# Performance work log

Hardware: AMD Instinct MI355X
Metric: run time of the kernel (lower is better)

## Reference

```python
import jax, jax.numpy as jnp
import numpy as np

B, C, H, W = 4, 128, 128, 128
NCLS = 80
NCONV = 2


def conv3x3(x, w, b):
    # x: [B,Cin,H,W], w: [Cout,Cin,3,3]
    y = jax.lax.conv_general_dilated(x, w, (1, 1), 'SAME',
                                     dimension_numbers=('NCHW', 'OIHW', 'NCHW'))
    return y + b[None, :, None, None]


def setup_inputs() -> dict:
    key = jax.random.key(0)
    ks = jax.random.split(key, 10)
    std = 0.01  # conv init std in the torch module
    prior_prob = 0.01
    bias_value = -np.log((1 - prior_prob) / prior_prob)
    inp = {
        'feature': jax.random.normal(ks[0], (B, C, H, W), jnp.float32),
        'targets': jax.random.uniform(ks[1], (B, NCLS, H, W), jnp.float32),
        'cls_w': std * jax.random.normal(ks[2], (NCONV, C, C, 3, 3), jnp.float32),
        'cls_b': jnp.zeros((NCONV, C), jnp.float32),
        'bbox_w': std * jax.random.normal(ks[3], (NCONV, C, C, 3, 3), jnp.float32),
        'bbox_b': jnp.zeros((NCONV, C), jnp.float32),
        'off_w': std * jax.random.normal(ks[4], (NCONV, C, C, 3, 3), jnp.float32),
        'off_b': jnp.zeros((NCONV, C), jnp.float32),
        'cls_score_w': std * jax.random.normal(ks[5], (NCLS, C, 3, 3), jnp.float32),
        'cls_score_b': jnp.full((NCLS,), bias_value, jnp.float32),
        'bbox_pred_w': std * jax.random.normal(ks[6], (2, C, 3, 3), jnp.float32),
        'bbox_pred_b': jnp.zeros((2,), jnp.float32),
        'center_off_w': std * jax.random.normal(ks[7], (2, C, 3, 3), jnp.float32),
        'center_off_b': jnp.zeros((2,), jnp.float32),
        'K': 100,
    }
    return inp


def centernet_forward(feature, targets, cls_w, cls_b, bbox_w, bbox_b, off_w, off_b,
                      cls_score_w, cls_score_b, bbox_pred_w, bbox_pred_b,
                      center_off_w, center_off_b, K):
    # ---- head: three conv+ReLU subnets + final 3x3 heads ----
    xc, xb, xo = feature, feature, feature
    for i in range(NCONV):
        xc = jax.nn.relu(conv3x3(xc, cls_w[i], cls_b[i]))
        xb = jax.nn.relu(conv3x3(xb, bbox_w[i], bbox_b[i]))
        xo = jax.nn.relu(conv3x3(xo, off_w[i], off_b[i]))
    logits = conv3x3(xc, cls_score_w, cls_score_b)      # [B,NCLS,H,W]
    wh = conv3x3(xb, bbox_pred_w, bbox_pred_b)          # [B,2,H,W]
    off = conv3x3(xo, center_off_w, center_off_b)       # [B,2,H,W]

    # ---- center focal loss (alpha=2, beta=4, reduction='sum') ----
    pos = (targets == 1.0).astype(logits.dtype)
    neg = (targets < 1.0).astype(logits.dtype)
    neg_w = jnp.power(1.0 - targets, 4.0)
    p = jax.nn.sigmoid(logits)
    log_p = jax.nn.log_sigmoid(logits)        # log(sigmoid(x))
    log_1mp = jax.nn.log_sigmoid(-logits)     # log(1 - sigmoid(x))
    pos_loss = log_p * jnp.square(1.0 - p) * pos
    neg_loss = log_1mp * jnp.square(p) * neg_w * neg
    loss = -(pos_loss.sum()) - (neg_loss.sum())

    # ---- decode: sigmoid + 3x3 maxpool pseudo-NMS + top-k + gather ----
    hm = p  # sigmoid heatmap
    hmax = jax.lax.reduce_window(hm, -jnp.inf, jax.lax.max,
                                 (1, 1, 3, 3), (1, 1, 1, 1), 'SAME')
    hm_nms = jnp.where(hmax == hm, hm, 0.0)
    scores, inds = jax.lax.top_k(hm_nms.reshape(B, -1), K)  # [B,K]
    hw = H * W
    clses = inds // hw                 # [B,K] int class ids
    sp = inds % hw                     # spatial index
    ys = (sp // W).astype(jnp.float32)
    xs = (sp % W).astype(jnp.float32)
    # gather wh/offset at peak locations
    wh_k = jnp.take_along_axis(wh.reshape(B, 2, hw), sp[:, None, :], axis=2)    # [B,2,K]
    off_k = jnp.take_along_axis(off.reshape(B, 2, hw), sp[:, None, :], axis=2)  # [B,2,K]
    cx = xs + off_k[:, 0]
    cy = ys + off_k[:, 1]
    w_, h_ = wh_k[:, 0], wh_k[:, 1]
    boxes = jnp.stack([cx - w_ / 2, cy - h_ / 2, cx + w_ / 2, cy + h_ / 2], axis=-1)  # [B,K,4]
    return boxes, scores, clses, loss


def reference(feature, targets, cls_w, cls_b, bbox_w, bbox_b, off_w, off_b,
              cls_score_w, cls_score_b, bbox_pred_w, bbox_pred_b,
              center_off_w, center_off_b, K):
    return centernet_forward(feature, targets, cls_w, cls_b, bbox_w, bbox_b,
                             off_w, off_b, cls_score_w, cls_score_b,
                             bbox_pred_w, bbox_pred_b, center_off_w,
                             center_off_b, K)
```

## Files before the change

kernel.cpp:

```cpp
#include <hip/hip_runtime.h>
#include <hip/hip_bf16.h>
#include <math.h>

#define B_    4
#define C_    128
#define H_    128
#define W_    128
#define HW_   (H_*W_)
#define NCLS_ 80
#define KTOP  100
#define CAPB  2048

typedef __attribute__((ext_vector_type(8)))  short bf16x8;
typedef __attribute__((ext_vector_type(16))) float f32x16;

#define WSTG_B     16384
#define WIMG_B     589824
#define NIMG       7
#define XROWB      144
#define XCOLS      130
#define XPITCH     (XCOLS * XROWB)
#define XSZ        ((size_t)16 * 130 * XPITCH)
#define XLDS_B     25920
#define LDS_TOT    (2 * XLDS_B)
#define ZERO_N     20512

__device__ __forceinline__ unsigned bf16_rne(float x) {
    unsigned u = __float_as_uint(x);
    return (u + 0x7FFFu + ((u >> 16) & 1u)) >> 16;
}
__device__ __forceinline__ void split2(float v0, float v1, unsigned& hiP, unsigned& loP) {
    unsigned h0 = bf16_rne(v0), h1 = bf16_rne(v1);
    float r0 = v0 - __uint_as_float(h0 << 16);
    float r1 = v1 - __uint_as_float(h1 << 16);
    unsigned l0 = bf16_rne(r0), l1 = bf16_rne(r1);
    hiP = h0 | (h1 << 16);
    loP = l0 | (l1 << 16);
}

#define MFMA32(a, bvec, c) __builtin_amdgcn_mfma_f32_32x32x16_bf16(a, bvec, c, 0, 0, 0)

__global__ __launch_bounds__(256) void init_k(char* __restrict__ xa, char* __restrict__ xb,
                                              unsigned* __restrict__ sm, float* __restrict__ loss)
{
    const int i = blockIdx.x * 256 + threadIdx.x;
    if (i < 16512) {
        char* buf = (i < 8256) ? xa : xb;
        const int j = (i < 8256) ? i : i - 8256;
        int R, col;
        if (j < 4160) {
            const int g = j / 260, rr = j % 260;
            R = g * 130 + ((rr < 130) ? 0 : 129);
            col = rr % 130;
        } else {
            const int q = j - 4160;
            const int g = q / 256, m = q % 256;
            R = g * 130 + 1 + (m >> 1);
            col = (m & 1) ? 129 : 0;
        }
        char* p = buf + ((size_t)R * XCOLS + col) * XROWB;
        #pragma unroll
        for (int k = 0; k < 9; k++) *(uint4*)(p + k * 16) = make_uint4(0, 0, 0, 0);
    } else {
        const int k = i - 16512;
        if (k < ZERO_N) sm[k] = 0u;
        if (k == ZERO_N) *loss = 0.f;
    }
}

struct WtArgs { const float* src[NIMG]; int cout[NIMG]; };

__global__ __launch_bounds__(256) void wtx_k(WtArgs a, unsigned short* wt)
{
    const int img = blockIdx.z;
    const int idx = blockIdx.x * 256 + threadIdx.x;
    const int h  = idx & 1;
    const int ks = (idx >> 1) & 1;
    const int r  = (idx >> 2) & 31;
    const int g  = (idx >> 7) & 3;
    const int st = idx >> 9;
    if (st >= 36) return;
    const int tap = st % 9, chunk = st / 9;
    const float* w = a.src[img];
    const int Cout = a.cout[img];
    const int cout = g * 32 + r;
    const int cin0 = chunk * 32 + ks * 16 + h * 8;
    float v[8];
    #pragma unroll
    for (int j = 0; j < 8; j++)
        v[j] = (cout < Cout) ? w[((size_t)cout * 128 + cin0 + j) * 9 + tap] : 0.f;
    unsigned hiW[4], loW[4];
    #pragma unroll
    for (int j = 0; j < 4; j++) split2(v[2 * j], v[2 * j + 1], hiW[j], loW[j]);
    char* dst = (char*)wt + (size_t)img * WIMG_B + (size_t)st * WSTG_B
              + g * 4096 + ks * 2048 + r * 32 + h * 16;
    *(uint4*)dst          = make_uint4(hiW[0], hiW[1], hiW[2], hiW[3]);
    *(uint4*)(dst + 1024) = make_uint4(loW[0], loW[1], loW[2], loW[3]);
}

template<int RELU, int XOUT>
__device__ __forceinline__ void conv_epilogue(
    f32x16 (&acc)[2][2], const bool* act,
    const float* bias, float* outf, char* outx, int Cout,
    int b, int x0, int y0, int wm, int wn, int kh, int l31)
{
    #pragma unroll
    for (int f = 0; f < 2; f++) {
        if (!act[f]) continue;
        if (XOUT == 0) {
            #pragma unroll
            for (int r = 0; r < 16; r++) {
                const int co = wm * 64 + f * 32 + 4 * kh + (r & 3) + 8 * (r >> 2);
                if (co < Cout) {
                    const float bv = bias[co];
                    #pragma unroll
                    for (int fn = 0; fn < 2; fn++) {
                        const int p = wn * 64 + fn * 32 + l31;
// ... 20 lines not shown
                    unsigned hiP, loP; split2(v0, v1, hiP, loP);
                    char* rowp = outx + ((size_t)((b * 4 + chunkO) * 130 + (y0 + (p >> 4) + 1)) * XCOLS
                                        + (x0 + (p & 15) + 1)) * XROWB;
                    *(unsigned*)(rowp + 2 * cij)      = hiP;
                    *(unsigned*)(rowp + 64 + 2 * cij) = loP;
                }
            }
        }
    }
}

#define WLOAD_(SLOT, SIDX) do {                                               \
    const char* wp_ = wb + (size_t)(SIDX) * WSTG_B;                           \
    _Pragma("unroll")                                                         \
    for (int f_ = 0; f_ < 2; f_++) {                                          \
        _Pragma("unroll")                                                     \
        for (int k_ = 0; k_ < 2; k_++) {                                      \
            wf[SLOT][f_ * 2 + k_]     = *(const bf16x8*)(wp_ + f_ * 4096 + k_ * 2048);        \
            wf[SLOT][4 + f_ * 2 + k_] = *(const bf16x8*)(wp_ + f_ * 4096 + k_ * 2048 + 1024); \
        }                                                                     \
    }                                                                         \
} while (0)

#define MFMA_TAP_(CUR, DOFF) do {                                             \
    _Pragma("unroll")                                                         \
    for (int ks = 0; ks < 2; ks++) {                                          \
        bf16x8 bh[2], bl[2];                                                  \
        _Pragma("unroll")                                                     \
        for (int fn = 0; fn < 2; fn++) {                                      \
            bh[fn] = *(const bf16x8*)(lds + baddr[fn] + (DOFF) + ks * 32);      \
            bl[fn] = *(const bf16x8*)(lds + baddr[fn] + (DOFF) + ks * 32 + 64); \
        }                                                                     \
        _Pragma("unroll")                                                     \
        for (int f = 0; f < 2; f++) if (act[f]) {                             \
            _Pragma("unroll")                                                 \
            for (int fn = 0; fn < 2; fn++)                                    \
                acc[f][fn] = MFMA32(wf[CUR][f * 2 + ks], bh[fn], acc[f][fn]); \
        }                                                                     \
        _Pragma("unroll")                                                     \
        for (int f = 0; f < 2; f++) if (act[f]) {                             \
            _Pragma("unroll")                                                 \
            for (int fn = 0; fn < 2; fn++)                                    \
                acc[f][fn] = MFMA32(wf[CUR][f * 2 + ks], bl[fn], acc[f][fn]); \
        }                                                                     \
        _Pragma("unroll")                                                     \
        for (int f = 0; f < 2; f++) if (act[f]) {                             \
            _Pragma("unroll")                                                 \
            for (int fn = 0; fn < 2; fn++)                                    \
                acc[f][fn] = MFMA32(wf[CUR][4 + f * 2 + ks], bh[fn], acc[f][fn]); \
        }                                                                     \
    }                                                                         \
} while (0)

template<int RELU, int XOUT>
__global__ __launch_bounds__(256, 2) void conv_f_k(
    const float* __restrict__ in, const unsigned short* __restrict__ wt,
    const float* __restrict__ bias, float* __restrict__ outf,
    char* __restrict__ outx, int Cout)
{
    __shared__ __align__(16) char lds[LDS_TOT];

    const int t    = threadIdx.x;
    const int lane = t & 63;
    const int wv   = t >> 6;
    const int wm   = wv >> 1;
    const int wn   = wv & 1;
    const int l31  = lane & 31;
    const int kh   = lane >> 5;

    const int bi = blockIdx.x;
    const int x0 = (bi & 7) << 4;
    const int y0 = ((bi >> 3) & 15) << 3;
    const int b  = bi >> 7;

    int baddr[2];
    #pragma unroll
    for (int fn = 0; fn < 2; fn++) {
        const int p = wn * 64 + fn * 32 + l31;
        baddr[fn] = ((p >> 4) * 18 + (p & 15)) * 144 + kh * 16;
    }
    bool act[2];
    #pragma unroll
    for (int f = 0; f < 2; f++) act[f] = (wm * 64 + f * 32) < Cout;

    const int wlane = ((lane & 31) << 5) | (kh << 4);
    const char* wb = (const char*)wt + wm * 8192 + wlane;

    f32x16 acc[2][2];
    #pragma unroll
    for (int i = 0; i < 2; i++)
        #pragma unroll
        for (int j = 0; j < 2; j++)
            #pragma unroll
            for (int r = 0; r < 16; r++) acc[i][j][r] = 0.f;

    const float* inb = in + (size_t)b * 128 * HW_;

    bf16x8 wf[2][8];
    WLOAD_(0, 0);

    float xa[12], xb[12];
    #define LOADX(ch) do {                                                    \
        _Pragma("unroll")                                                     \
        for (int it = 0; it < 12; it++) {                                     \
            const int idx = t + it * 256;                                     \
            const int pl = idx & 15, cp = (idx >> 4) & 15, ph = idx >> 8;     \
            const int pos = ph * 16 + pl;                                     \
            float v0 = 0.f, v1 = 0.f;                                         \
            if (pos < 180) {                                                  \
                const int hy = pos / 18, hx = pos - hy * 18;                  \
                const int gy = y0 - 1 + hy, gx = x0 - 1 + hx;                 \
                if ((unsigned)gy < 128u && (unsigned)gx < 128u) {             \
                    const float* p0 = inb + (size_t)((ch) * 32 + 2 * cp) * HW_ \
                                          + gy * 128 + gx;                    \
                    v0 = p0[0]; v1 = p0[HW_];                                 \
                }                                                             \
            }                                                                 \
            xa[it] = v0; xb[it] = v1;                                         \
        }                                                                     \
    } while (0)

    #define STOREX(bufsel) do {                                               \
        _Pragma("unroll")                                                     \
        for (int it = 0; it < 12; it++) {                                     \
            const int idx = t + it * 256;                                     \
            const int pl = idx & 15, cp = (idx >> 4) & 15, ph = idx >> 8;     \
            const int pos = ph * 16 + pl;                                     \
            if (pos < 180) {                                                  \
                unsigned hiP, loP; split2(xa[it], xb[it], hiP, loP);          \
                *(unsigned*)(lds + (bufsel) * XLDS_B + pos * 144 + 4 * cp)      = hiP; \
                *(unsigned*)(lds + (bufsel) * XLDS_B + pos * 144 + 64 + 4 * cp) = loP; \
            }                                                                 \
        }                                                                     \
    } while (0)

    LOADX(0);
    STOREX(0);
    __syncthreads();

    #define TAPF(CH, TAP, CUR, NXT) do {                                      \
        if ((CH) * 9 + (TAP) + 1 < 36) WLOAD_(NXT, (CH) * 9 + (TAP) + 1);     \
        MFMA_TAP_(CUR, (((TAP) / 3) * 18 + ((TAP) % 3)) * 144 + ((CH) & 1) * XLDS_B); \
    } while (0)

    #define CHUNKF(CH, SA, SB) do {                                           \
        TAPF(CH, 0, SA, SB); TAPF(CH, 1, SB, SA); TAPF(CH, 2, SA, SB);        \
        TAPF(CH, 3, SB, SA); TAPF(CH, 4, SA, SB); TAPF(CH, 5, SB, SA);        \
        if ((CH) < 3) LOADX((CH) + 1);                                        \
        TAPF(CH, 6, SA, SB); TAPF(CH, 7, SB, SA); TAPF(CH, 8, SA, SB);        \
        if ((CH) < 3) { STOREX(((CH) + 1) & 1); __syncthreads(); }            \
    } while (0)

    CHUNKF(0, 0, 1);
    CHUNKF(1, 1, 0);
    CHUNKF(2, 0, 1);
    CHUNKF(3, 1, 0);

    #undef LOADX
    #undef STOREX
    #undef TAPF
    #undef CHUNKF
    conv_epilogue<RELU, XOUT>(acc, act, bias, outf, outx, Cout, b, x0, y0, wm, wn, kh, l31);
}

template<int RELU, int XOUT>
__global__ __launch_bounds__(256, 2) void conv_x_k(
    const char* __restrict__ xin, const unsigned short* __restrict__ wt,
    const float* __restrict__ bias, float* __restrict__ outf,
    char* __restrict__ outx, int Cout)
{
    __shared__ __align__(16) char lds[LDS_TOT];

    const int t    = threadIdx.x;
    const int lane = t & 63;
    const int wv   = t >> 6;
    const int wm   = wv >> 1;
    const int wn   = wv & 1;
    const int l31  = lane & 31;
    const int kh   = lane >> 5;

    const int bi = blockIdx.x;
    const int x0 = (bi & 7) << 4;
    const int y0 = ((bi >> 3) & 15) << 3;
    const int b  = bi >> 7;

    int baddr[2];
    #pragma unroll
    for (int fn = 0; fn < 2; fn++) {
        const int p = wn * 64 + fn * 32 + l31;
        baddr[fn] = (p >> 4) * 2592 + (p & 15) * 144 + kh * 16;
    }
    bool act[2];
    #pragma unroll
    for (int f = 0; f < 2; f++) act[f] = (wm * 64 + f * 32) < Cout;

    const int wlane = ((lane & 31) << 5) | (kh << 4);
    const char* wb = (const char*)wt + wm * 8192 + wlane;

    f32x16 acc[2][2];
    #pragma unroll
    for (int i = 0; i < 2; i++)
        #pragma unroll
        for (int j = 0; j < 2; j++)
            #pragma unroll
            for (int r = 0; r < 16; r++) acc[i][j][r] = 0.f;

    bf16x8 wf[2][8];
    WLOAD_(0, 0);

    {
        const size_t rowbase = ((size_t)((b * 4 + 0) * 130 + y0) * XCOLS + x0) * XROWB;
        #pragma unroll
        for (int gg = 0; gg < 5; gg++) {
            const int g = wv * 5 + gg;
            const int hy = g >> 1, i = g & 1;
            __builtin_amdgcn_global_load_lds(
                (const __attribute__((address_space(1))) unsigned*)
                    (xin + rowbase + (size_t)hy * XPITCH + i * 1024 + lane * 16),
                (__attribute__((address_space(3))) unsigned*)(lds + hy * 2592 + i * 1024),
                16, 0, 0);
        }
        for (int u = t; u < 340; u += 256) {
            const int hy = u / 34;
            const int off = 2048 + (u % 34) * 16;
            uint4 v = *(const uint4*)(xin + rowbase + (size_t)hy * XPITCH + off);
            *(uint4*)(lds + hy * 2592 + off) = v;
        }
    }
    __syncthreads();

    #define TAPX(CH, TAP, CUR, NXT) do {                                      \
        if ((CH) * 9 + (TAP) + 1 < 36) WLOAD_(NXT, (CH) * 9 + (TAP) + 1);     \
        MFMA_TAP_(CUR, ((TAP) / 3) * 2592 + ((TAP) % 3) * 144 + ((CH) & 1) * XLDS_B); \
    } while (0)

    #define CHUNKX(CH, SA, SB) do {                                           \
        uint4 tl0_, tl1_; bool h1_ = false;                                   \
        const int xd_ = (((CH) + 1) & 1) * XLDS_B;                            \
        if ((CH) < 3) {                                                       \
            const size_t rowb1_ = ((size_t)((b * 4 + (CH) + 1) * 130 + y0) * XCOLS + x0) * XROWB; \
            _Pragma("unroll")                                                 \
            for (int gg = 0; gg < 5; gg++) {                                  \
                const int g = wv * 5 + gg;                                    \
                const int hy = g >> 1, ii = g & 1;                            \
                __builtin_amdgcn_global_load_lds(                             \
                    (const __attribute__((address_space(1))) unsigned*)       \
                        (xin + rowb1_ + (size_t)hy * XPITCH + ii * 1024 + lane * 16), \
                    (__attribute__((address_space(3))) unsigned*)(lds + xd_ + hy * 2592 + ii * 1024), \
                    16, 0, 0);                                                \
            }                                                                 \
            {                                                                 \
                const int hy = t / 34, off = 2048 + (t % 34) * 16;            \
                tl0_ = *(const uint4*)(xin + rowb1_ + (size_t)hy * XPITCH + off); \
            }                                                                 \
            h1_ = (t < 84);                                                   \
            if (h1_) {                                                        \
                const int u = t + 256;                                        \
                const int hy = u / 34, off = 2048 + (u % 34) * 16;            \
                tl1_ = *(const uint4*)(xin + rowb1_ + (size_t)hy * XPITCH + off); \
            }                                                                 \
        }                                                                     \
        TAPX(CH, 0, SA, SB); TAPX(CH, 1, SB, SA); TAPX(CH, 2, SA, SB);        \
        TAPX(CH, 3, SB, SA); TAPX(CH, 4, SA, SB); TAPX(CH, 5, SB, SA);        \
        TAPX(CH, 6, SA, SB); TAPX(CH, 7, SB, SA); TAPX(CH, 8, SA, SB);        \
        if ((CH) < 3) {                                                       \
            {                                                                 \
                const int hy = t / 34, off = 2048 + (t % 34) * 16;            \
                *(uint4*)(lds + xd_ + hy * 2592 + off) = tl0_;                \
            }                                                                 \
            if (h1_) {                                                        \
                const int u = t + 256;                                        \
                const int hy = u / 34, off = 2048 + (u % 34) * 16;            \
                *(uint4*)(lds + xd_ + hy * 2592 + off) = tl1_;                \
            }                                                                 \
            __syncthreads();                                                  \
        }                                                                     \
    } while (0)

    CHUNKX(0, 0, 1);
    CHUNKX(1, 1, 0);
    CHUNKX(2, 0, 1);
    CHUNKX(3, 1, 0);

    #undef TAPX
    #undef CHUNKX
    conv_epilogue<RELU, XOUT>(acc, act, bias, outf, outx, Cout, b, x0, y0, wm, wn, kh, l31);
}

__global__ __launch_bounds__(256) void conv2out_k(
    const float* __restrict__ in, const float* __restrict__ w,
    const float* __restrict__ bias, float* __restrict__ out)
{
    __shared__ float ws[128 * 9 * 2];
    const int t = threadIdx.x;
    for (int i = t; i < 2304; i += 256) {
        const int co = i & 1, tap = (i >> 1) % 9, ci = i / 18;
        ws[i] = w[(size_t)co * 1152 + ci * 9 + tap];
    }
    __syncthreads();

    const int b  = blockIdx.y;
    const int y  = (blockIdx.x >> 3) * 16 + (t >> 4);
    const int x  = (blockIdx.x & 7) * 16 + (t & 15);
    const float* inb = in + (size_t)b * 128 * HW_ + y * 128 + x;

    float a0 = bias[0], a1 = bias[1];
    #pragma unroll 2
    for (int ci = 0; ci < 128; ci++) {
        const float* p  = inb + (size_t)ci * HW_;
        const float* wp = ws + ci * 18;
        #pragma unroll
        for (int tap = 0; tap < 9; tap++) {
            const int dy = tap / 3 - 1, dx = tap % 3 - 1;
            const int yy = y + dy, xx = x + dx;
            float v = 0.f;
            if ((unsigned)yy < 128u && (unsigned)xx < 128u) v = p[dy * 128 + dx];
            a0 = fmaf(v, wp[tap * 2 + 0], a0);
            a1 = fmaf(v, wp[tap * 2 + 1], a1);
        }
    }
    out[((size_t)b * 2 + 0) * HW_ + y * 128 + x] = a0;
    out[((size_t)b * 2 + 1) * HW_ + y * 128 + x] = a1;
}

__global__ __launch_bounds__(256) void lnh_k(
    const float* __restrict__ L, const float* __restrict__ targets,
    float* __restrict__ loss_out, unsigned* __restrict__ keys,
    unsigned* __restrict__ hist)
{
    __shared__ unsigned h[2048];
    for (int j = threadIdx.x; j < 2048; j += 256) h[j] = 0;
    __syncthreads();

    const int per_b = NCLS_ * HW_;
    const int b = blockIdx.y;
    const float* Lb = L + (size_t)b * per_b;
    const float* Tb = targets + (size_t)b * per_b;
    unsigned* kb = keys + (size_t)b * per_b;

    float sum = 0.f;
    for (int i = blockIdx.x * 256 + threadIdx.x; i < per_b; i += gridDim.x * 256) {
        const float x = Lb[i];
        const float t = Tb[i];
        const float e   = expf(-fabsf(x));
        const float inv = 1.f / (1.f + e);
        const float lp  = log1pf(e);
        const bool  xe  = (x >= 0.f);
        const float p   = xe ? inv : e * inv;
        const float lsp = xe ? -lp : (x - lp);
        const float lsn = lsp - x;
        float om = 1.f - t;
        float nw = om * om; nw *= nw;
        const float omp = 1.f - p;
        if (t == 1.0f)     sum -= lsp * omp * omp;
        else if (t < 1.0f) sum -= lsn * p * p * nw;

        const int sp = i & (HW_ - 1);
        const int y = sp >> 7, xq = sp & 127;
        const float* plane = Lb + (i - sp);
        const int ym = (y > 0) ? y - 1 : 0,   yp = (y < 127) ? y + 1 : 127;
        const int xm = (xq > 0) ? xq - 1 : 0, xp = (xq < 127) ? xq + 1 : 127;
        const float* r0 = plane + ym * 128;
        const float* r1 = plane + y  * 128;
        const float* r2 = plane + yp * 128;
        float m = fmaxf(fmaxf(fmaxf(r0[xm], r0[xq]), fmaxf(r0[xp], r1[xm])),
                 fmaxf(fmaxf(x, r1[xp]),
                 fmaxf(fmaxf(r2[xm], r2[xq]), r2[xp])));
        const float em   = expf(-fabsf(m));
        const float invm = 1.f / (1.f + em);
        const float pm   = (m >= 0.f) ? invm : em * invm;
        const unsigned key = (__float_as_uint(p) == __float_as_uint(pm)) ? __float_as_uint(p) : 0u;
        kb[i] = key;
        if (key) atomicAdd(&h[key >> 21], 1u);
    }

// ... 166 lines not shown
        ok[rank] = kk; oi[rank] = ii;
    }
    __syncthreads();

    if (threadIdx.x < KTOP) {
        int r = threadIdx.x;
        unsigned ind = oi[r];
        float score = __uint_as_float(ok[r]);
        int cls = (int)(ind / HW_);
        int sp  = (int)(ind % HW_);
        float ysf = (float)(sp >> 7);
        float xsf = (float)(sp & 127);
        float w0 = wh[((size_t)b * 2 + 0) * HW_ + sp];
        float h0 = wh[((size_t)b * 2 + 1) * HW_ + sp];
        float o0 = off[((size_t)b * 2 + 0) * HW_ + sp];
        float o1 = off[((size_t)b * 2 + 1) * HW_ + sp];
        float cx = xsf + o0;
        float cy = ysf + o1;
        float* boxes  = out;
        float* scores = out + (size_t)B_ * KTOP * 4;
        float* clses  = out + (size_t)B_ * KTOP * 5;
        boxes[((size_t)b * KTOP + r) * 4 + 0] = cx - w0 * 0.5f;
        boxes[((size_t)b * KTOP + r) * 4 + 1] = cy - h0 * 0.5f;
        boxes[((size_t)b * KTOP + r) * 4 + 2] = cx + w0 * 0.5f;
        boxes[((size_t)b * KTOP + r) * 4 + 3] = cy + h0 * 0.5f;
        scores[b * KTOP + r] = score;
        clses[b * KTOP + r]  = (float)cls;
    }
}

extern "C" void kernel_launch(void* const* d_in, const int* in_sizes, int n_in,
                              void* d_out, int out_size, void* d_ws, size_t ws_size,
                              hipStream_t stream)
{
    const float* feature      = (const float*)d_in[0];
    const float* targets      = (const float*)d_in[1];
    const float* cls_w        = (const float*)d_in[2];
    const float* cls_b        = (const float*)d_in[3];
    const float* bbox_w       = (const float*)d_in[4];
    const float* bbox_b       = (const float*)d_in[5];
    const float* off_w        = (const float*)d_in[6];
    const float* off_b        = (const float*)d_in[7];
    const float* cls_score_w  = (const float*)d_in[8];
    const float* cls_score_b  = (const float*)d_in[9];
    const float* bbox_pred_w  = (const float*)d_in[10];
    const float* bbox_pred_b  = (const float*)d_in[11];
    const float* center_off_w = (const float*)d_in[12];
    const float* center_off_b = (const float*)d_in[13];
    float* out = (float*)d_out;

    const size_t L_BYTES  = (size_t)B_ * NCLS_ * HW_ * 4;
    const size_t P_BYTES  = (size_t)B_ * 2 * HW_ * 4;
    const size_t WT_BYTES = (size_t)NIMG * WIMG_B;

    char* ws = (char*)d_ws;
    const size_t lw = (size_t)C_ * C_ * 9;
    float* loss_ptr = out + (size_t)B_ * KTOP * 6;

    char* XA = ws;
    char* XB = ws + XSZ;
    float* L   = (float*)(ws + 2 * XSZ);
    float* WH  = (float*)(ws + 2 * XSZ + L_BYTES);
    float* OFF = (float*)(ws + 2 * XSZ + L_BYTES + P_BYTES);
    unsigned short* WT = (unsigned short*)(ws + 2 * XSZ + L_BYTES + 2 * P_BYTES);
    unsigned* sm = (unsigned*)(ws + 2 * XSZ + L_BYTES + 2 * P_BYTES + WT_BYTES);
    float* Bf = (float*)XB;
    unsigned* keys = (unsigned*)XB;

    unsigned* hist1 = sm;
    unsigned* hist2 = sm + 4 * 2048;
    unsigned* hist3 = sm + 8 * 2048;
    unsigned* bin1  = sm + 8 * 2048 + 4 * 1024;
    unsigned* gt1   = bin1 + 4;
    unsigned* pfx2  = bin1 + 8;
    unsigned* gt2   = bin1 + 12;
    unsigned* Tk    = bin1 + 16;
    unsigned* gt3   = bin1 + 20;
    unsigned* cntA  = bin1 + 24;
    unsigned* cntB  = bin1 + 28;
    uint2*    listA = (uint2*)(bin1 + 32);
    unsigned* listB = (unsigned*)(bin1 + 32 + 2 * B_ * KTOP);

    WtArgs wa;
    wa.src[0] = cls_w;        wa.cout[0] = 128;
    wa.src[1] = bbox_w;       wa.cout[1] = 128;
    wa.src[2] = off_w;        wa.cout[2] = 128;
    wa.src[3] = cls_w + lw;   wa.cout[3] = 128;
    wa.src[4] = bbox_w + lw;  wa.cout[4] = 128;
    wa.src[5] = off_w + lw;   wa.cout[5] = 128;
    wa.src[6] = cls_score_w;  wa.cout[6] = NCLS_;

    init_k<<<145, 256, 0, stream>>>(XA, XB, sm, loss_ptr);
    wtx_k<<<dim3(72, 1, NIMG), 256, 0, stream>>>(wa, WT);

    #define WIMG(i) (WT + (size_t)(i) * (WIMG_B / 2))

    conv_f_k<1, 1><<<512, 256, 0, stream>>>(feature, WIMG(0), cls_b,       nullptr, XA, 128);
    conv_x_k<1, 1><<<512, 256, 0, stream>>>(XA,      WIMG(3), cls_b + C_,  nullptr, XB, 128);
    conv_x_k<0, 0><<<512, 256, 0, stream>>>(XB,      WIMG(6), cls_score_b, L, nullptr, NCLS_);
    conv_f_k<1, 1><<<512, 256, 0, stream>>>(feature, WIMG(1), bbox_b,      nullptr, XA, 128);
    conv_x_k<1, 0><<<512, 256, 0, stream>>>(XA,      WIMG(4), bbox_b + C_, Bf, nullptr, 128);
    conv2out_k<<<dim3(64, 4), 256, 0, stream>>>(Bf, bbox_pred_w, bbox_pred_b, WH);
    conv_f_k<1, 1><<<512, 256, 0, stream>>>(feature, WIMG(2), off_b,       nullptr, XA, 128);
    conv_x_k<1, 0><<<512, 256, 0, stream>>>(XA,      WIMG(5), off_b + C_,  Bf, nullptr, 128);
    conv2out_k<<<dim3(64, 4), 256, 0, stream>>>(Bf, center_off_w, center_off_b, OFF);

    lnh_k<<<dim3(512, B_), 256, 0, stream>>>(L, targets, loss_ptr, keys, hist1);

    dim3 hgrid(512, B_);
    scan_k<2048, 1><<<B_, 256, 0, stream>>>(hist1, nullptr, nullptr, bin1, gt1);
    hist2_k<<<hgrid, 256, 0, stream>>>(keys, bin1, hist2);
    scan_k<2048, 2><<<B_, 256, 0, stream>>>(hist2, bin1, gt1, pfx2, gt2);
    hist3_k<<<hgrid, 256, 0, stream>>>(keys, pfx2, hist3);
    scan_k<1024, 3><<<B_, 256, 0, stream>>>(hist3, pfx2, gt2, Tk, gt3);
    select_k<<<hgrid, 256, 0, stream>>>(keys, Tk, cntA, cntB, listA, listB);

    finalize_k<<<B_, 128, 0, stream>>>(cntA, cntB, listA, listB, Tk, WH, OFF, out);
}
```

Measured before the change: 577.4 us.

## Batch the three subnet convs into single wide launches with separate activation buffers

Result: faster. 548.1 us (-5.1%).

```diff
diff --git a/kernel.cpp b/kernel.cpp
--- a/kernel.cpp
+++ b/kernel.cpp
@@ -40,13 +40,14 @@
 
 #define MFMA32(a, bvec, c) __builtin_amdgcn_mfma_f32_32x32x16_bf16(a, bvec, c, 0, 0, 0)
 
-__global__ __launch_bounds__(256) void init_k(char* __restrict__ xa, char* __restrict__ xb,
+__global__ __launch_bounds__(256) void init_k(char* __restrict__ xbase, int nbuf,
                                               unsigned* __restrict__ sm, float* __restrict__ loss)
 {
     const int i = blockIdx.x * 256 + threadIdx.x;
-    if (i < 16512) {
-        char* buf = (i < 8256) ? xa : xb;
-        const int j = (i < 8256) ? i : i - 8256;
+    const int nb = nbuf * 8256;
+    if (i < nb) {
+        char* buf = xbase + (size_t)(i / 8256) * XSZ;
+        const int j = i % 8256;
         int R, col;
         if (j < 4160) {
             const int g = j / 260, rr = j % 260;
@@ -62,7 +63,7 @@
         #pragma unroll
         for (int k = 0; k < 9; k++) *(uint4*)(p + k * 16) = make_uint4(0, 0, 0, 0);
     } else {
-        const int k = i - 16512;
+        const int k = i - nb;
         if (k < ZERO_N) sm[k] = 0u;
         if (k == ZERO_N) *loss = 0.f;
     }
@@ -189,116 +190,232 @@
     }                                                                         \
 } while (0)
 
+#define CONVF_SETUP()                                                         \
+    __shared__ __align__(16) char lds[LDS_TOT];                               \
+    const int t    = threadIdx.x;                                             \
+    const int lane = t & 63;                                                  \
+    const int wv   = t >> 6;                                                  \
+    const int wm   = wv >> 1;                                                 \
+    const int wn   = wv & 1;                                                  \
+    const int l31  = lane & 31;                                               \
+    const int kh   = lane >> 5;                                               \
+    const int bi = blockIdx.x;                                                \
+    const int x0 = (bi & 7) << 4;                                             \
+    const int y0 = ((bi >> 3) & 15) << 3;                                     \
+    const int b  = bi >> 7;                                                   \
+    int baddr[2];                                                             \
+    _Pragma("unroll")                                                         \
+    for (int fn = 0; fn < 2; fn++) {                                          \
+        const int p = wn * 64 + fn * 32 + l31;                                \
+        baddr[fn] = ((p >> 4) * 18 + (p & 15)) * 144 + kh * 16;               \
+    }                                                                         \
+    const int wlane = ((lane & 31) << 5) | (kh << 4);                         \
+    f32x16 acc[2][2];                                                         \
+    _Pragma("unroll")                                                         \
+    for (int i_ = 0; i_ < 2; i_++)                                            \
+        _Pragma("unroll")                                                     \
+        for (int j_ = 0; j_ < 2; j_++)                                        \
+            _Pragma("unroll")                                                 \
+            for (int r_ = 0; r_ < 16; r_++) acc[i_][j_][r_] = 0.f;
+
+#define LOADX_F(ch) do {                                                      \
+    _Pragma("unroll")                                                         \
+    for (int it = 0; it < 12; it++) {                                         \
+        const int idx = t + it * 256;                                         \
+        const int pl = idx & 15, cp = (idx >> 4) & 15, ph = idx >> 8;         \
+        const int pos = ph * 16 + pl;                                         \
+        float v0 = 0.f, v1 = 0.f;                                             \
+        if (pos < 180) {                                                      \
+            const int hy = pos / 18, hx = pos - hy * 18;                      \
+            const int gy = y0 - 1 + hy, gx = x0 - 1 + hx;                     \
+            if ((unsigned)gy < 128u && (unsigned)gx < 128u) {                 \
+                const float* p0 = inb + (size_t)((ch) * 32 + 2 * cp) * HW_    \
+                                      + gy * 128 + gx;                        \
+                v0 = p0[0]; v1 = p0[HW_];                                     \
+            }                                                                 \
+        }                                                                     \
+        xa[it] = v0; xb[it] = v1;                                             \
+    }                                                                         \
+} while (0)
+
+#define STOREX_F(bufsel) do {                                                 \
+    _Pragma("unroll")                                                         \
+    for (int it = 0; it < 12; it++) {                                         \
+        const int idx = t + it * 256;                                         \
+        const int pl = idx & 15, cp = (idx >> 4) & 15, ph = idx >> 8;         \
+        const int pos = ph * 16 + pl;                                         \
+        if (pos < 180) {                                                      \
+            unsigned hiP, loP; split2(xa[it], xb[it], hiP, loP);              \
+            *(unsigned*)(lds + (bufsel) * XLDS_B + pos * 144 + 4 * cp)      = hiP; \
+            *(unsigned*)(lds + (bufsel) * XLDS_B + pos * 144 + 64 + 4 * cp) = loP; \
+        }                                                                     \
+    }                                                                         \
+} while (0)
+
+#define TAPF_(CH, TAP, CUR, NXT) do {                                         \
+    if ((CH) * 9 + (TAP) + 1 < 36) WLOAD_(NXT, (CH) * 9 + (TAP) + 1);         \
+    MFMA_TAP_(CUR, (((TAP) / 3) * 18 + ((TAP) % 3)) * 144 + ((CH) & 1) * XLDS_B); \
+} while (0)
+
+#define CHUNKF_(CH, SA, SB) do {                                              \
+    TAPF_(CH, 0, SA, SB); TAPF_(CH, 1, SB, SA); TAPF_(CH, 2, SA, SB);         \
+    TAPF_(CH, 3, SB, SA); TAPF_(CH, 4, SA, SB); TAPF_(CH, 5, SB, SA);         \
+    if ((CH) < 3) LOADX_F((CH) + 1);                                          \
+    TAPF_(CH, 6, SA, SB); TAPF_(CH, 7, SB, SA); TAPF_(CH, 8, SA, SB);         \
+    if ((CH) < 3) { STOREX_F(((CH) + 1) & 1); __syncthreads(); }              \
+} while (0)
+
+#define CONVF_MAIN()                                                          \
+    bf16x8 wf[2][8];                                                          \
+    WLOAD_(0, 0);                                                             \
+    float xa[12], xb[12];                                                     \
+    LOADX_F(0);                                                               \
+    STOREX_F(0);                                                              \
+    __syncthreads();                                                          \
+    CHUNKF_(0, 0, 1);                                                         \
+    CHUNKF_(1, 1, 0);                                                         \
+    CHUNKF_(2, 0, 1);                                                         \
+    CHUNKF_(3, 1, 0);
+
 template<int RELU, int XOUT>
 __global__ __launch_bounds__(256, 2) void conv_f_k(
     const float* __restrict__ in, const unsigned short* __restrict__ wt,
     const float* __restrict__ bias, float* __restrict__ outf,
     char* __restrict__ outx, int Cout)
 {
-    __shared__ __align__(16) char lds[LDS_TOT];
-
-    const int t    = threadIdx.x;
-    const int lane = t & 63;
-    const int wv   = t >> 6;
-    const int wm   = wv >> 1;
-    const int wn   = wv & 1;
-    const int l31  = lane & 31;
-    const int kh   = lane >> 5;
-
-    const int bi = blockIdx.x;
-    const int x0 = (bi & 7) << 4;
-    const int y0 = ((bi >> 3) & 15) << 3;
-    const int b  = bi >> 7;
-
-    int baddr[2];
-    #pragma unroll
-    for (int fn = 0; fn < 2; fn++) {
-        const int p = wn * 64 + fn * 32 + l31;
-        baddr[fn] = ((p >> 4) * 18 + (p & 15)) * 144 + kh * 16;
-    }
+    CONVF_SETUP();
     bool act[2];
     #pragma unroll
     for (int f = 0; f < 2; f++) act[f] = (wm * 64 + f * 32) < Cout;
-
-    const int wlane = ((lane & 31) << 5) | (kh << 4);
     const char* wb = (const char*)wt + wm * 8192 + wlane;
-
-    f32x16 acc[2][2];
-    #pragma unroll
-    for (int i = 0; i < 2; i++)
-        #pragma unroll
-        for (int j = 0; j < 2; j++)
-            #pragma unroll
-            for (int r = 0; r < 16; r++) acc[i][j][r] = 0.f;
-
     const float* inb = in + (size_t)b * 128 * HW_;
-
-    bf16x8 wf[2][8];
-    WLOAD_(0, 0);
-
-    float xa[12], xb[12];
-    #define LOADX(ch) do {                                                    \
+    CONVF_MAIN();
+    conv_epilogue<RELU, XOUT>(acc, act, bias, outf, outx, Cout, b, x0, y0, wm, wn, kh, l31);
+}
+
+struct F3Args { const unsigned short* wt[3]; const float* bias[3]; char* outx[3]; };
+
+__global__ __launch_bounds__(256, 2) void convF3_k(const float* __restrict__ in, F3Args a)
+{
+    const int ty = blockIdx.y;
+    const unsigned short* wt = a.wt[ty];
+    const float* bias = a.bias[ty];
+    char* outx = a.outx[ty];
+
+    CONVF_SETUP();
+    bool act[2]; act[0] = true; act[1] = true;
+    const char* wb = (const char*)wt + wm * 8192 + wlane;
+    const float* inb = in + (size_t)b * 128 * HW_;
+    CONVF_MAIN();
+    conv_epilogue<1, 1>(acc, act, bias, nullptr, outx, 128, b, x0, y0, wm, wn, kh, l31);
+}
+
+#define CONVX_SETUP()                                                         \
+    __shared__ __align__(16) char lds[LDS_TOT];                               \
+    const int t    = threadIdx.x;                                             \
+    const int lane = t & 63;                                                  \
+    const int wv   = t >> 6;                                                  \
+    const int wm   = wv >> 1;                                                 \
+    const int wn   = wv & 1;                                                  \
+    const int l31  = lane & 31;                                               \
+    const int kh   = lane >> 5;                                               \
+    const int bi = blockIdx.x;                                                \
+    const int x0 = (bi & 7) << 4;                                             \
+    const int y0 = ((bi >> 3) & 15) << 3;                                     \
+    const int b  = bi >> 7;                                                   \
+    int baddr[2];                                                             \
+    _Pragma("unroll")                                                         \
+    for (int fn = 0; fn < 2; fn++) {                                          \
+        const int p = wn * 64 + fn * 32 + l31;                                \
+        baddr[fn] = (p >> 4) * 2592 + (p & 15) * 144 + kh * 16;               \
+    }                                                                         \
+    const int wlane = ((lane & 31) << 5) | (kh << 4);                         \
+    f32x16 acc[2][2];                                                         \
+    _Pragma("unroll")                                                         \
+    for (int i_ = 0; i_ < 2; i_++)                                            \
         _Pragma("unroll")                                                     \
-        for (int it = 0; it < 12; it++) {                                     \
-            const int idx = t + it * 256;                                     \
-            const int pl = idx & 15, cp = (idx >> 4) & 15, ph = idx >> 8;     \
-            const int pos = ph * 16 + pl;                                     \
-            float v0 = 0.f, v1 = 0.f;                                         \
-            if (pos < 180) {                                                  \
-                const int hy = pos / 18, hx = pos - hy * 18;                  \
-                const int gy = y0 - 1 + hy, gx = x0 - 1 + hx;                 \
-                if ((unsigned)gy < 128u && (unsigned)gx < 128u) {             \
-                    const float* p0 = inb + (size_t)((ch) * 32 + 2 * cp) * HW_ \
-                                          + gy * 128 + gx;                    \
-                    v0 = p0[0]; v1 = p0[HW_];                                 \
-                }                                                             \
-            }                                                                 \
-            xa[it] = v0; xb[it] = v1;                                         \
-        }                                                                     \
-    } while (0)
-
-    #define STOREX(bufsel) do {                                               \
+        for (int j_ = 0; j_ < 2; j_++)                                        \
+            _Pragma("unroll")                                                 \
+            for (int r_ = 0; r_ < 16; r_++) acc[i_][j_][r_] = 0.f;
+
+#define CONVX_PROLOG()                                                        \
+    {                                                                         \
+        const size_t rowbase = ((size_t)((b * 4 + 0) * 130 + y0) * XCOLS + x0) * XROWB; \
         _Pragma("unroll")                                                     \
-        for (int it = 0; it < 12; it++) {                                     \
-            const int idx = t + it * 256;                                     \
-            const int pl = idx & 15, cp = (idx >> 4) & 15, ph = idx >> 8;     \
-            const int pos = ph * 16 + pl;                                     \
-            if (pos < 180) {                                                  \
-                unsigned hiP, loP; split2(xa[it], xb[it], hiP, loP);          \
-                *(unsigned*)(lds + (bufsel) * XLDS_B + pos * 144 + 4 * cp)      = hiP; \
-                *(unsigned*)(lds + (bufsel) * XLDS_B + pos * 144 + 64 + 4 * cp) = loP; \
-            }                                                                 \
-        }                                                                     \
-    } while (0)
-
-    LOADX(0);
-    STOREX(0);
-    __syncthreads();
-
-    #define TAPF(CH, TAP, CUR, NXT) do {                                      \
-        if ((CH) * 9 + (TAP) + 1 < 36) WLOAD_(NXT, (CH) * 9 + (TAP) + 1);     \
-        MFMA_TAP_(CUR, (((TAP) / 3) * 18 + ((TAP) % 3)) * 144 + ((CH) & 1) * XLDS_B); \
-    } while (0)
-
-    #define CHUNKF(CH, SA, SB) do {                                           \
-        TAPF(CH, 0, SA, SB); TAPF(CH, 1, SB, SA); TAPF(CH, 2, SA, SB);        \
-        TAPF(CH, 3, SB, SA); TAPF(CH, 4, SA, SB); TAPF(CH, 5, SB, SA);        \
-        if ((CH) < 3) LOADX((CH) + 1);                                        \
-        TAPF(CH, 6, SA, SB); TAPF(CH, 7, SB, SA); TAPF(CH, 8, SA, SB);        \
-        if ((CH) < 3) { STOREX(((CH) + 1) & 1); __syncthreads(); }            \
-    } while (0)
-
-    CHUNKF(0, 0, 1);
-    CHUNKF(1, 1, 0);
-    CHUNKF(2, 0, 1);
-    CHUNKF(3, 1, 0);
-
-    #undef LOADX
-    #undef STOREX
-    #undef TAPF
-    #undef CHUNKF
-    conv_epilogue<RELU, XOUT>(acc, act, bias, outf, outx, Cout, b, x0, y0, wm, wn, kh, l31);
-}
+        for (int gg = 0; gg < 5; gg++) {                                      \
+            const int g = wv * 5 + gg;                                        \
+            const int hy = g >> 1, i = g & 1;                                 \
+            __builtin_amdgcn_global_load_lds(                                 \
+                (const __attribute__((address_space(1))) unsigned*)           \
+                    (xin + rowbase + (size_t)hy * XPITCH + i * 1024 + lane * 16), \
+                (__attribute__((address_space(3))) unsigned*)(lds + hy * 2592 + i * 1024), \
+                16, 0, 0);                                                    \
+        }                                                                     \
+        for (int u = t; u < 340; u += 256) {                                  \
+            const int hy = u / 34;                                            \
+            const int off = 2048 + (u % 34) * 16;                             \
+            uint4 v = *(const uint4*)(xin + rowbase + (size_t)hy * XPITCH + off); \
+            *(uint4*)(lds + hy * 2592 + off) = v;                             \
+        }                                                                     \
+    }                                                                         \
+    __syncthreads();
+
+#define TAPX_(CH, TAP, CUR, NXT) do {                                         \
+    if ((CH) * 9 + (TAP) + 1 < 36) WLOAD_(NXT, (CH) * 9 + (TAP) + 1);         \
+    MFMA_TAP_(CUR, ((TAP) / 3) * 2592 + ((TAP) % 3) * 144 + ((CH) & 1) * XLDS_B); \
+} while (0)
+
+#define CHUNKX_(CH, SA, SB) do {                                              \
+    uint4 tl0_, tl1_; bool h1_ = false;                                       \
+    const int xd_ = (((CH) + 1) & 1) * XLDS_B;                                \
+    if ((CH) < 3) {                                                           \
+        const size_t rowb1_ = ((size_t)((b * 4 + (CH) + 1) * 130 + y0) * XCOLS + x0) * XROWB; \
+        _Pragma("unroll")                                                     \
+        for (int gg = 0; gg < 5; gg++) {                                      \
+            const int g = wv * 5 + gg;                                        \
+            const int hy = g >> 1, ii = g & 1;                                \
+            __builtin_amdgcn_global_load_lds(                                 \
+                (const __attribute__((address_space(1))) unsigned*)           \
+                    (xin + rowb1_ + (size_t)hy * XPITCH + ii * 1024 + lane * 16), \
+                (__attribute__((address_space(3))) unsigned*)(lds + xd_ + hy * 2592 + ii * 1024), \
+                16, 0, 0);                                                    \
+        }                                                                     \
+        {                                                                     \
+            const int hy = t / 34, off = 2048 + (t % 34) * 16;                \
+            tl0_ = *(const uint4*)(xin + rowb1_ + (size_t)hy * XPITCH + off); \
+        }                                                                     \
+        h1_ = (t < 84);                                                       \
+        if (h1_) {                                                            \
+            const int u = t + 256;                                            \
+            const int hy = u / 34, off = 2048 + (u % 34) * 16;                \
+            tl1_ = *(const uint4*)(xin + rowb1_ + (size_t)hy * XPITCH + off); \
+        }                                                                     \
+    }                                                                         \
+    TAPX_(CH, 0, SA, SB); TAPX_(CH, 1, SB, SA); TAPX_(CH, 2, SA, SB);         \
+    TAPX_(CH, 3, SB, SA); TAPX_(CH, 4, SA, SB); TAPX_(CH, 5, SB, SA);         \
+    TAPX_(CH, 6, SA, SB); TAPX_(CH, 7, SB, SA); TAPX_(CH, 8, SA, SB);         \
+    if ((CH) < 3) {                                                           \
+        {                                                                     \
+            const int hy = t / 34, off = 2048 + (t % 34) * 16;                \
+            *(uint4*)(lds + xd_ + hy * 2592 + off) = tl0_;                    \
+        }                                                                     \
+        if (h1_) {                                                            \
+            const int u = t + 256;                                            \
+            const int hy = u / 34, off = 2048 + (u % 34) * 16;                \
+            *(uint4*)(lds + xd_ + hy * 2592 + off) = tl1_;                    \
+        }                                                                     \
+        __syncthreads();                                                      \
+    }                                                                         \
+} while (0)
+
+#define CONVX_MAIN()                                                          \
+    bf16x8 wf[2][8];                                                          \
+    WLOAD_(0, 0);                                                             \
+    CONVX_PROLOG();                                                           \
+    CHUNKX_(0, 0, 1);                                                         \
+    CHUNKX_(1, 1, 0);                                                         \
+    CHUNKX_(2, 0, 1);                                                         \
+    CHUNKX_(3, 1, 0);
 
 template<int RELU, int XOUT>
 __global__ __launch_bounds__(256, 2) void conv_x_k(
@@ -306,127 +423,40 @@
     const float* __restrict__ bias, float* __restrict__ outf,
     char* __restrict__ outx, int Cout)
 {
-    __shared__ __align__(16) char lds[LDS_TOT];
-
-    const int t    = threadIdx.x;
-    const int lane = t & 63;
-    const int wv   = t >> 6;
-    const int wm   = wv >> 1;
-    const int wn   = wv & 1;
-    const int l31  = lane & 31;
-    const int kh   = lane >> 5;
-
-    const int bi = blockIdx.x;
-    const int x0 = (bi & 7) << 4;
-    const int y0 = ((bi >> 3) & 15) << 3;
-    const int b  = bi >> 7;
-
-    int baddr[2];
-    #pragma unroll
-    for (int fn = 0; fn < 2; fn++) {
-        const int p = wn * 64 + fn * 32 + l31;
-        baddr[fn] = (p >> 4) * 2592 + (p & 15) * 144 + kh * 16;
-    }
+    CONVX_SETUP();
     bool act[2];
     #pragma unroll
     for (int f = 0; f < 2; f++) act[f] = (wm * 64 + f * 32) < Cout;
-
-    const int wlane = ((lane & 31) << 5) | (kh << 4);
     const char* wb = (const char*)wt + wm * 8192 + wlane;
-
-    f32x16 acc[2][2];
-    #pragma unroll
-    for (int i = 0; i < 2; i++)
-        #pragma unroll
-        for (int j = 0; j < 2; j++)
-            #pragma unroll
-            for (int r = 0; r < 16; r++) acc[i][j][r] = 0.f;
-
-    bf16x8 wf[2][8];
-    WLOAD_(0, 0);
-
-    {
-        const size_t rowbase = ((size_t)((b * 4 + 0) * 130 + y0) * XCOLS + x0) * XROWB;
-        #pragma unroll
-        for (int gg = 0; gg < 5; gg++) {
-            const int g = wv * 5 + gg;
-            const int hy = g >> 1, i = g & 1;
-            __builtin_amdgcn_global_load_lds(
-                (const __attribute__((address_space(1))) unsigned*)
-                    (xin + rowbase + (size_t)hy * XPITCH + i * 1024 + lane * 16),
-                (__attribute__((address_space(3))) unsigned*)(lds + hy * 2592 + i * 1024),
-                16, 0, 0);
-        }
-        for (int u = t; u < 340; u += 256) {
-            const int hy = u / 34;
-            const int off = 2048 + (u % 34) * 16;
-            uint4 v = *(const uint4*)(xin + rowbase + (size_t)hy * XPITCH + off);
-            *(uint4*)(lds + hy * 2592 + off) = v;
-        }
-    }
-    __syncthreads();
-
-    #define TAPX(CH, TAP, CUR, NXT) do {                                      \
-        if ((CH) * 9 + (TAP) + 1 < 36) WLOAD_(NXT, (CH) * 9 + (TAP) + 1);     \
-        MFMA_TAP_(CUR, ((TAP) / 3) * 2592 + ((TAP) % 3) * 144 + ((CH) & 1) * XLDS_B); \
-    } while (0)
-
-    #define CHUNKX(CH, SA, SB) do {                                           \
-        uint4 tl0_, tl1_; bool h1_ = false;                                   \
-        const int xd_ = (((CH) + 1) & 1) * XLDS_B;                            \
-        if ((CH) < 3) {                                                       \
-            const size_t rowb1_ = ((size_t)((b * 4 + (CH) + 1) * 130 + y0) * XCOLS + x0) * XROWB; \
-            _Pragma("unroll")                                                 \
-            for (int gg = 0; gg < 5; gg++) {                                  \
-                const int g = wv * 5 + gg;                                    \
-                const int hy = g >> 1, ii = g & 1;                            \
-                __builtin_amdgcn_global_load_lds(                             \
-                    (const __attribute__((address_space(1))) unsigned*)       \
-                        (xin + rowb1_ + (size_t)hy * XPITCH + ii * 1024 + lane * 16), \
-                    (__attribute__((address_space(3))) unsigned*)(lds + xd_ + hy * 2592 + ii * 1024), \
-                    16, 0, 0);                                                \
-            }                                                                 \
-            {                                                                 \
-                const int hy = t / 34, off = 2048 + (t % 34) * 16;            \
-                tl0_ = *(const uint4*)(xin + rowb1_ + (size_t)hy * XPITCH + off); \
-            }                                                                 \
-            h1_ = (t < 84);                                                   \
-            if (h1_) {                                                        \
-                const int u = t + 256;                                        \
-                const int hy = u / 34, off = 2048 + (u % 34) * 16;            \
-                tl1_ = *(const uint4*)(xin + rowb1_ + (size_t)hy * XPITCH + off); \
-            }                                                                 \
-        }                                                                     \
-        TAPX(CH, 0, SA, SB); TAPX(CH, 1, SB, SA); TAPX(CH, 2, SA, SB);        \
-        TAPX(CH, 3, SB, SA); TAPX(CH, 4, SA, SB); TAPX(CH, 5, SB, SA);        \
-        TAPX(CH, 6, SA, SB); TAPX(CH, 7, SB, SA); TAPX(CH, 8, SA, SB);        \
-        if ((CH) < 3) {                                                       \
-            {                                                                 \
-                const int hy = t / 34, off = 2048 + (t % 34) * 16;            \
-                *(uint4*)(lds + xd_ + hy * 2592 + off) = tl0_;                \
-            }                                                                 \
-            if (h1_) {                                                        \
-                const int u = t + 256;                                        \
-                const int hy = u / 34, off = 2048 + (u % 34) * 16;            \
-                *(uint4*)(lds + xd_ + hy * 2592 + off) = tl1_;                \
-            }                                                                 \
-            __syncthreads();                                                  \
-        }                                                                     \
-    } while (0)
-
-    CHUNKX(0, 0, 1);
-    CHUNKX(1, 1, 0);
-    CHUNKX(2, 0, 1);
-    CHUNKX(3, 1, 0);
-
-    #undef TAPX
-    #undef CHUNKX
+    CONVX_MAIN();
     conv_epilogue<RELU, XOUT>(acc, act, bias, outf, outx, Cout, b, x0, y0, wm, wn, kh, l31);
 }
 
-__global__ __launch_bounds__(256) void conv2out_k(
-    const float* __restrict__ in, const float* __restrict__ w,
-    const float* __restrict__ bias, float* __restrict__ out)
+struct X3Args {
+    const char* xin[3]; const unsigned short* wt[3]; const float* bias[3];
+    float* outf[3]; char* outx[3]; int xout[3];
+};
+
+__global__ __launch_bounds__(256, 2) void convX3_k(X3Args a)
+{
+    const int ty = blockIdx.y;
+    const char* xin = a.xin[ty];
+    const unsigned short* wt = a.wt[ty];
+    const float* bias = a.bias[ty];
+    float* outf = a.outf[ty];
+    char* outx = a.outx[ty];
+    const int xo = a.xout[ty];
+
+    CONVX_SETUP();
+    bool act[2]; act[0] = true; act[1] = true;
+    const char* wb = (const char*)wt + wm * 8192 + wlane;
+    CONVX_MAIN();
+    if (xo) conv_epilogue<1, 1>(acc, act, bias, nullptr, outx, 128, b, x0, y0, wm, wn, kh, l31);
+    else    conv_epilogue<1, 0>(acc, act, bias, outf, nullptr, 128, b, x0, y0, wm, wn, kh, l31);
+}
+
+__device__ __forceinline__ void conv2out_body(
+    const float* in, const float* w, const float* bias, float* out)
 {
     __shared__ float ws[128 * 9 * 2];
     const int t = threadIdx.x;
@@ -458,6 +488,23 @@
     }
     out[((size_t)b * 2 + 0) * HW_ + y * 128 + x] = a0;
     out[((size_t)b * 2 + 1) * HW_ + y * 128 + x] = a1;
+}
+
+__global__ __launch_bounds__(256) void conv2out_k(
+    const float* __restrict__ in, const float* __restrict__ w,
+    const float* __restrict__ bias, float* __restrict__ out)
+{
+    conv2out_body(in, w, bias, out);
+}
+
+__global__ __launch_bounds__(256) void conv2out2_k(
+    const float* in0, const float* in1,
+    const float* w0, const float* w1,
+    const float* b0, const float* b1,
+    float* out0, float* out1)
+{
+    const int z = blockIdx.z;
+    conv2out_body(z ? in1 : in0, z ? w1 : w0, z ? b1 : b0, z ? out1 : out0);
 }
 
 __global__ __launch_bounds__(256) void lnh_k(
@@ -730,34 +777,11 @@
     const size_t L_BYTES  = (size_t)B_ * NCLS_ * HW_ * 4;
     const size_t P_BYTES  = (size_t)B_ * 2 * HW_ * 4;
     const size_t WT_BYTES = (size_t)NIMG * WIMG_B;
+    const size_t SM_BYTES = (size_t)1 << 18;
 
     char* ws = (char*)d_ws;
     const size_t lw = (size_t)C_ * C_ * 9;
     float* loss_ptr = out + (size_t)B_ * KTOP * 6;
-
-    char* XA = ws;
-    char* XB = ws + XSZ;
-    float* L   = (float*)(ws + 2 * XSZ);
-    float* WH  = (float*)(ws + 2 * XSZ + L_BYTES);
-    float* OFF = (float*)(ws + 2 * XSZ + L_BYTES + P_BYTES);
-    unsigned short* WT = (unsigned short*)(ws + 2 * XSZ + L_BYTES + 2 * P_BYTES);
-    unsigned* sm = (unsigned*)(ws + 2 * XSZ + L_BYTES + 2 * P_BYTES + WT_BYTES);
-    float* Bf = (float*)XB;
-    unsigned* keys = (unsigned*)XB;
-
-    unsigned* hist1 = sm;
-    unsigned* hist2 = sm + 4 * 2048;
-    unsigned* hist3 = sm + 8 * 2048;
-    unsigned* bin1  = sm + 8 * 2048 + 4 * 1024;
-    unsigned* gt1   = bin1 + 4;
-    unsigned* pfx2  = bin1 + 8;
-    unsigned* gt2   = bin1 + 12;
-    unsigned* Tk    = bin1 + 16;
-    unsigned* gt3   = bin1 + 20;
-    unsigned* cntA  = bin1 + 24;
-    unsigned* cntB  = bin1 + 28;
-    uint2*    listA = (uint2*)(bin1 + 32);
-    unsigned* listB = (unsigned*)(bin1 + 32 + 2 * B_ * KTOP);
 
     WtArgs wa;
     wa.src[0] = cls_w;        wa.cout[0] = 128;
@@ -768,30 +792,119 @@
     wa.src[5] = off_w + lw;   wa.cout[5] = 128;
     wa.src[6] = cls_score_w;  wa.cout[6] = NCLS_;
 
-    init_k<<<145, 256, 0, stream>>>(XA, XB, sm, loss_ptr);
-    wtx_k<<<dim3(72, 1, NIMG), 256, 0, stream>>>(wa, WT);
+    const size_t FUSED_NEED = 6 * XSZ + 2 * P_BYTES + WT_BYTES + SM_BYTES;
 
     #define WIMG(i) (WT + (size_t)(i) * (WIMG_B / 2))
 
-    conv_f_k<1, 1><<<512, 256, 0, stream>>>(feature, WIMG(0), cls_b,       nullptr, XA, 128);
-    conv_x_k<1, 1><<<512, 256, 0, stream>>>(XA,      WIMG(3), cls_b + C_,  nullptr, XB, 128);
-    conv_x_k<0, 0><<<512, 256, 0, stream>>>(XB,      WIMG(6), cls_score_b, L, nullptr, NCLS_);
-    conv_f_k<1, 1><<<512, 256, 0, stream>>>(feature, WIMG(1), bbox_b,      nullptr, XA, 128);
-    conv_x_k<1, 0><<<512, 256, 0, stream>>>(XA,      WIMG(4), bbox_b + C_, Bf, nullptr, 128);
-    conv2out_k<<<dim3(64, 4), 256, 0, stream>>>(Bf, bbox_pred_w, bbox_pred_b, WH);
-    conv_f_k<1, 1><<<512, 256, 0, stream>>>(feature, WIMG(2), off_b,       nullptr, XA, 128);
-    conv_x_k<1, 0><<<512, 256, 0, stream>>>(XA,      WIMG(5), off_b + C_,  Bf, nullptr, 128);
-    conv2out_k<<<dim3(64, 4), 256, 0, stream>>>(Bf, center_off_w, center_off_b, OFF);
-
-    lnh_k<<<dim3(512, B_), 256, 0, stream>>>(L, targets, loss_ptr, keys, hist1);
-
-    dim3 hgrid(512, B_);
-    scan_k<2048, 1><<<B_, 256, 0, stream>>>(hist1, nullptr, nullptr, bin1, gt1);
-    hist2_k<<<hgrid, 256, 0, stream>>>(keys, bin1, hist2);
-    scan_k<2048, 2><<<B_, 256, 0, stream>>>(hist2, bin1, gt1, pfx2, gt2);
-    hist3_k<<<hgrid, 256, 0, stream>>>(keys, pfx2, hist3);
-    scan_k<1024, 3><<<B_, 256, 0, stream>>>(hist3, pfx2, gt2, Tk, gt3);
-    select_k<<<hgrid, 256, 0, stream>>>(keys, Tk, cntA, cntB, listA, listB);
-
-    finalize_k<<<B_, 128, 0, stream>>>(cntA, cntB, listA, listB, Tk, WH, OFF, out);
-}
+    if (ws_size >= FUSED_NEED) {
+        char* XA0 = ws;
+        char* XA1 = ws + XSZ;
+        char* XA2 = ws + 2 * XSZ;
+        char* XB  = ws + 3 * XSZ;
+        float* Bfb = (float*)(ws + 4 * XSZ);
+        float* Bfo = (float*)(ws + 5 * XSZ);
+        float* L   = (float*)XA0;
+        unsigned* keys = (unsigned*)XA1;
+        float* WH  = (float*)(ws + 6 * XSZ);
+        float* OFF = (float*)(ws + 6 * XSZ + P_BYTES);
+        unsigned short* WT = (unsigned short*)(ws + 6 * XSZ + 2 * P_BYTES);
+        unsigned* sm = (unsigned*)(ws + 6 * XSZ + 2 * P_BYTES + WT_BYTES);
+
+        unsigned* hist1 = sm;
+        unsigned* hist2 = sm + 4 * 2048;
+        unsigned* hist3 = sm + 8 * 2048;
+        unsigned* bin1  = sm + 8 * 2048 + 4 * 1024;
+        unsigned* gt1   = bin1 + 4;
+        unsigned* pfx2  = bin1 + 8;
+        unsigned* gt2   = bin1 + 12;
+        unsigned* Tk    = bin1 + 16;
+        unsigned* gt3   = bin1 + 20;
+        unsigned* cntA  = bin1 + 24;
+        unsigned* cntB  = bin1 + 28;
+        uint2*    listA = (uint2*)(bin1 + 32);
+        unsigned* listB = (unsigned*)(bin1 + 32 + 2 * B_ * KTOP);
+
+        init_k<<<210, 256, 0, stream>>>(XA0, 4, sm, loss_ptr);
+        wtx_k<<<dim3(72, 1, NIMG), 256, 0, stream>>>(wa, WT);
+
+        F3Args f3;
+        f3.wt[0] = WIMG(0); f3.bias[0] = cls_b;  f3.outx[0] = XA0;
+        f3.wt[1] = WIMG(1); f3.bias[1] = bbox_b; f3.outx[1] = XA1;
+        f3.wt[2] = WIMG(2); f3.bias[2] = off_b;  f3.outx[2] = XA2;
+        convF3_k<<<dim3(512, 3), 256, 0, stream>>>(feature, f3);
+
+        X3Args x3;
+        x3.xin[0] = XA0; x3.wt[0] = WIMG(3); x3.bias[0] = cls_b + C_;
+        x3.outf[0] = nullptr; x3.outx[0] = XB; x3.xout[0] = 1;
+        x3.xin[1] = XA1; x3.wt[1] = WIMG(4); x3.bias[1] = bbox_b + C_;
+        x3.outf[1] = Bfb; x3.outx[1] = nullptr; x3.xout[1] = 0;
+        x3.xin[2] = XA2; x3.wt[2] = WIMG(5); x3.bias[2] = off_b + C_;
+        x3.outf[2] = Bfo; x3.outx[2] = nullptr; x3.xout[2] = 0;
+        convX3_k<<<dim3(512, 3), 256, 0, stream>>>(x3);
+
+        conv_x_k<0, 0><<<512, 256, 0, stream>>>(XB, WIMG(6), cls_score_b, L, nullptr, NCLS_);
+        conv2out2_k<<<dim3(64, 4, 2), 256, 0, stream>>>(
+            Bfb, Bfo, bbox_pred_w, center_off_w, bbox_pred_b, center_off_b, WH, OFF);
+
+        lnh_k<<<dim3(512, B_), 256, 0, stream>>>(L, targets, loss_ptr, keys, hist1);
+
+        dim3 hgrid(512, B_);
+        scan_k<2048, 1><<<B_, 256, 0, stream>>>(hist1, nullptr, nullptr, bin1, gt1);
+        hist2_k<<<hgrid, 256, 0, stream>>>(keys, bin1, hist2);
+        scan_k<2048, 2><<<B_, 256, 0, stream>>>(hist2, bin1, gt1, pfx2, gt2);
+        hist3_k<<<hgrid, 256, 0, stream>>>(keys, pfx2, hist3);
+        scan_k<1024, 3><<<B_, 256, 0, stream>>>(hist3, pfx2, gt2, Tk, gt3);
+        select_k<<<hgrid, 256, 0, stream>>>(keys, Tk, cntA, cntB, listA, listB);
+
+        finalize_k<<<B_, 128, 0, stream>>>(cntA, cntB, listA, listB, Tk, WH, OFF, out);
+    } else {
+        char* XA = ws;
+        char* XB = ws + XSZ;
+        float* L   = (float*)(ws + 2 * XSZ);
+        float* WH  = (float*)(ws + 2 * XSZ + L_BYTES);
+        float* OFF = (float*)(ws + 2 * XSZ + L_BYTES + P_BYTES);
+        unsigned short* WT = (unsigned short*)(ws + 2 * XSZ + L_BYTES + 2 * P_BYTES);
+        unsigned* sm = (unsigned*)(ws + 2 * XSZ + L_BYTES + 2 * P_BYTES + WT_BYTES);
+        float* Bf = (float*)XB;
+        unsigned* keys = (unsigned*)XB;
+
+        unsigned* hist1 = sm;
+        unsigned* hist2 = sm + 4 * 2048;
+        unsigned* hist3 = sm + 8 * 2048;
+        unsigned* bin1  = sm + 8 * 2048 + 4 * 1024;
+        unsigned* gt1   = bin1 + 4;
+        unsigned* pfx2  = bin1 + 8;
+        unsigned* gt2   = bin1 + 12;
+        unsigned* Tk    = bin1 + 16;
+        unsigned* gt3   = bin1 + 20;
+        unsigned* cntA  = bin1 + 24;
+        unsigned* cntB  = bin1 + 28;
+        uint2*    listA = (uint2*)(bin1 + 32);
+        unsigned* listB = (unsigned*)(bin1 + 32 + 2 * B_ * KTOP);
+
+        init_k<<<145, 256, 0, stream>>>(XA, 2, sm, loss_ptr);
+        wtx_k<<<dim3(72, 1, NIMG), 256, 0, stream>>>(wa, WT);
+
+        conv_f_k<1, 1><<<512, 256, 0, stream>>>(feature, WIMG(0), cls_b,       nullptr, XA, 128);
+        conv_x_k<1, 1><<<512, 256, 0, stream>>>(XA,      WIMG(3), cls_b + C_,  nullptr, XB, 128);
+        conv_x_k<0, 0><<<512, 256, 0, stream>>>(XB,      WIMG(6), cls_score_b, L, nullptr, NCLS_);
+        conv_f_k<1, 1><<<512, 256, 0, stream>>>(feature, WIMG(1), bbox_b,      nullptr, XA, 128);
+        conv_x_k<1, 0><<<512, 256, 0, stream>>>(XA,      WIMG(4), bbox_b + C_, Bf, nullptr, 128);
+        conv2out_k<<<dim3(64, 4), 256, 0, stream>>>(Bf, bbox_pred_w, bbox_pred_b, WH);
+        conv_f_k<1, 1><<<512, 256, 0, stream>>>(feature, WIMG(2), off_b,       nullptr, XA, 128);
+        conv_x_k<1, 0><<<512, 256, 0, stream>>>(XA,      WIMG(5), off_b + C_,  Bf, nullptr, 128);
+        conv2out_k<<<dim3(64, 4), 256, 0, stream>>>(Bf, center_off_w, center_off_b, OFF);
+
+        lnh_k<<<dim3(512, B_), 256, 0, stream>>>(L, targets, loss_ptr, keys, hist1);
+
+        dim3 hgrid(512, B_);
+        scan_k<2048, 1><<<B_, 256, 0, stream>>>(hist1, nullptr, nullptr, bin1, gt1);
+        hist2_k<<<hgrid, 256, 0, stream>>>(keys, bin1, hist2);
+        scan_k<2048, 2><<<B_, 256, 0, stream>>>(hist2, bin1, gt1, pfx2, gt2);
+        hist3_k<<<hgrid, 256, 0, stream>>>(keys, pfx2, hist3);
+        scan_k<1024, 3><<<B_, 256, 0, stream>>>(hist3, pfx2, gt2, Tk, gt3);
+        select_k<<<hgrid, 256, 0, stream>>>(keys, Tk, cntA, cntB, listA, listB);
+
+        finalize_k<<<B_, 128, 0, stream>>>(cntA, cntB, listA, listB, Tk, WH, OFF, out);
+    }
+}
```
